# Optimization experiments

Hardware: AMD Instinct MI355X
Metric: run time of the kernel (lower is better)

## Reference

```python
import jax, jax.numpy as jnp
import numpy as np

HEAD = 12
HEAD_DIM = 64  # dim // head = 768 // 12


def setup_inputs() -> dict:
    key = jax.random.key(0)
    k1, k2, k3 = jax.random.split(key, 3)
    B, N, D = 4, 2048, 768
    scale = 1.0 / np.sqrt(D)
    return {
        "x": jax.random.normal(k1, (B, N, D), dtype=jnp.float32),
        "w_qkv": jax.random.normal(k2, (D, 3 * D), dtype=jnp.float32) * scale,
        "w_proj": jax.random.normal(k3, (D, D), dtype=jnp.float32) * scale,
        "b_proj": jnp.zeros((D,), dtype=jnp.float32),
    }


def reference(x, w_qkv, w_proj, b_proj):
    B, N, D = x.shape
    qkv = x @ w_qkv  # [B, N, 3D]
    q, k, v = jnp.split(qkv, 3, axis=-1)
    # [B, H, N, k]
    def heads(t):
        return t.reshape(B, N, HEAD, HEAD_DIM).transpose(0, 2, 1, 3)
    q, k, v = heads(q), heads(k), heads(v)
    attn = jnp.einsum("bhnd,bhmd->bhnm", q, k) / jnp.sqrt(jnp.float32(HEAD_DIM))
    attn_prob = jax.nn.softmax(attn, axis=-1)  # dropout p=0.0 -> identity
    out = jnp.einsum("bhnm,bhmd->bhnd", attn_prob, v)
    out = out.transpose(0, 2, 1, 3).reshape(B, N, D)
    return out @ w_proj + b_proj
```

## Files before the change

kernel.cpp:

```cpp
#include <hip/hip_runtime.h>

typedef unsigned short u16;
typedef unsigned int u32;
typedef u16 u16x4 __attribute__((ext_vector_type(4)));
typedef u16 u16x8 __attribute__((ext_vector_type(8)));
typedef u32 u32x2 __attribute__((ext_vector_type(2)));
typedef u32 u32x4 __attribute__((ext_vector_type(4)));
typedef __bf16 bf16x8 __attribute__((ext_vector_type(8)));
typedef float f32x4 __attribute__((ext_vector_type(4)));
typedef float f32x16 __attribute__((ext_vector_type(16)));

#define MFMA16 __builtin_amdgcn_mfma_f32_16x16x32_bf16
#define MFMA32 __builtin_amdgcn_mfma_f32_32x32x16_bf16

__device__ __forceinline__ u16 f2bf(float f) {
  return __builtin_bit_cast(u16, (__bf16)f);
}

__device__ __forceinline__ u32 pk2bf(float a, float b) {
  return (u32)__builtin_bit_cast(u16, (__bf16)a) |
         ((u32)__builtin_bit_cast(u16, (__bf16)b) << 16);
}

__device__ __forceinline__ u32x2 swap32(u32 a, u32 b, int hi) {
#if __has_builtin(__builtin_amdgcn_permlane32_swap)
  (void)hi;
  return __builtin_amdgcn_permlane32_swap(a, b, false, false);
#else
  u32 sa = (u32)__shfl_xor((int)a, 32), sb = (u32)__shfl_xor((int)b, 32);
  u32x2 r;
  r[0] = hi ? sb : a;
  r[1] = hi ? b : sa;
  return r;
#endif
}

__device__ __forceinline__ void gload_lds16(const void* g, void* l) {
  __builtin_amdgcn_global_load_lds(
      (const __attribute__((address_space(1))) u32*)g,
      (__attribute__((address_space(3))) u32*)l, 16, 0, 0);
}

__global__ __launch_bounds__(256)
void prepass_kernel(const float* __restrict__ x, u16* __restrict__ xb,
                    const float* __restrict__ wq, u16* __restrict__ wqT,
                    const float* __restrict__ wp, u16* __restrict__ wpT) {
  __shared__ float t[32][33];
  const int bid = blockIdx.x, tid = threadIdx.x;
  if (bid < 6144) {
    const int i = bid * 256 + tid;
    float4 v = reinterpret_cast<const float4*>(x)[i];
    u16x4 o;
    o[0] = f2bf(v.x); o[1] = f2bf(v.y); o[2] = f2bf(v.z); o[3] = f2bf(v.w);
    reinterpret_cast<u16x4*>(xb)[i] = o;
    return;
  }
  const float* w;
  u16* wt;
  int N, b2;
  if (bid < 7872) { b2 = bid - 6144; w = wq; wt = wqT; N = 2304; }
  else            { b2 = bid - 7872; w = wp; wt = wpT; N = 768; }
  const int K = 768;
  const int bk = (b2 % 24) * 32, bn = (b2 / 24) * 32;
  const int xx = tid & 31, yy = tid >> 5;
#pragma unroll
  for (int j = 0; j < 32; j += 8)
    t[yy + j][xx] = w[(size_t)(bk + yy + j) * N + bn + xx];
  __syncthreads();
#pragma unroll
  for (int j = 0; j < 32; j += 8)
    wt[(size_t)(bn + yy + j) * K + bk + xx] = f2bf(t[xx][yy + j]);
}

#define QSCALE 0.18033688011112042f

template <int NTOT, int EPI, int NT>
__global__ __launch_bounds__(256)
void gemm_bf16_kernel(const u16* __restrict__ A, const u16* __restrict__ BT,
                      u16* __restrict__ qo, u16* __restrict__ ko,
                      u16* __restrict__ vt, float* __restrict__ outF,
                      const float* __restrict__ bias) {
  __shared__ u16 sh[16384];
  u16* As = sh;
  u16* Bs = sh + 8192;
  const int tid = threadIdx.x;
  const int l = tid & 63, w = tid >> 6;
  const int lr = l & 15, lg = l >> 4;
  const int swz = (blockIdx.x & 7) * (8 * NT) + (blockIdx.x >> 3);
  const int mtile = swz / NT;
  const int ntile = swz % NT;
  const int mbase = mtile * 128, nbase = ntile * 128;
  const int wr = (w >> 1) * 64, wc = (w & 1) * 64;

  f32x4 acc[4][4] = {};

  for (int k0 = 0; k0 < 768; k0 += 64) {
#pragma unroll
    for (int i = 0; i < 4; ++i) {
      const int c = w * 64 + i * 256 + l;
      const int row = c >> 3, c16 = c & 7;
      const int sc = c16 ^ (row & 7);
      gload_lds16(A + (size_t)(mbase + row) * 768 + k0 + sc * 8,
                  &As[(size_t)(w * 64 + i * 256) * 8]);
      gload_lds16(BT + (size_t)(nbase + row) * 768 + k0 + sc * 8,
                  &Bs[(size_t)(w * 64 + i * 256) * 8]);
    }
    __syncthreads();
#pragma unroll
    for (int ks = 0; ks < 2; ++ks) {
      bf16x8 af[4], bfr[4];
#pragma unroll
      for (int m = 0; m < 4; ++m) {
        const int row = wr + m * 16 + lr;
        const int byte = (row * 128 + ks * 64 + lg * 16) ^ ((row & 7) << 4);
        af[m] = *reinterpret_cast<const bf16x8*>((const char*)As + byte);
      }
#pragma unroll
      for (int n = 0; n < 4; ++n) {
        const int row = wc + n * 16 + lr;
        const int byte = (row * 128 + ks * 64 + lg * 16) ^ ((row & 7) << 4);
        bfr[n] = *reinterpret_cast<const bf16x8*>((const char*)Bs + byte);
      }
#pragma unroll
      for (int m = 0; m < 4; ++m)
#pragma unroll
        for (int n = 0; n < 4; ++n)
          acc[m][n] = MFMA16(af[m], bfr[n], acc[m][n], 0, 0, 0);
    }
    __syncthreads();
  }

  if (EPI == 0 && ntile >= 12) {
    u16* vts = sh;
#pragma unroll
    for (int m = 0; m < 4; ++m)
#pragma unroll
      for (int n = 0; n < 4; ++n)
#pragma unroll
        for (int r = 0; r < 4; ++r) {
          const int col = wc + n * 16 + lr;
          const int row = wr + m * 16 + lg * 4 + r;
          const int byte = col * 256 + ((row * 2) ^ ((col & 7) << 4));
          *reinterpret_cast<u16*>((char*)vts + byte) = f2bf(acc[m][n][r]);
        }
    __syncthreads();
    const int b2 = mbase >> 11, nn0 = mbase & 2047;
#pragma unroll
    for (int i = 0; i < 8; ++i) {
      const int idx = i * 256 + tid;
      const int col = idx >> 4, u = idx & 15;
      u16x8 vv = *reinterpret_cast<u16x8*>(
          (char*)vts + (col * 256 + ((u * 16) ^ ((col & 7) << 4))));
      const int cg = nbase - 1536 + col;
      const int hh = cg >> 6, dd = cg & 63;
      *reinterpret_cast<u16x8*>(
          vt + (((size_t)(b2 * 12 + hh)) * 64 + dd) * 2048 + nn0 + u * 8) = vv;
    }
    return;
  }

#pragma unroll
  for (int m = 0; m < 4; ++m) {
#pragma unroll
    for (int n = 0; n < 4; ++n) {
#pragma unroll
      for (int r = 0; r < 4; ++r) {
        const int row = mbase + wr + m * 16 + lg * 4 + r;
        const int col = nbase + wc + n * 16 + lr;
        float val = acc[m][n][r];
        if (EPI == 0) {
          const int w2 = col / 768;
          const int c2 = col - w2 * 768;
          const int hh = c2 >> 6, dd = c2 & 63;
          const int b2 = row >> 11, nn = row & 2047;
          u16* dst = (w2 == 0) ? qo : ko;
          if (w2 == 0) val *= QSCALE;
          dst[(((size_t)(b2 * 12 + hh)) * 2048 + nn) * 64 + dd] = f2bf(val);
        } else {
          outF[(size_t)row * NTOT + col] = val + bias[col];
        }
      }
    }
  }
}

__global__ __launch_bounds__(256)
void flash_attn32_kernel(const u16* __restrict__ qb, const u16* __restrict__ kb,
                         const u16* __restrict__ vtb, u16* __restrict__ ao) {
  __shared__ u16 sh[32768];
  const int tid = threadIdx.x, w = tid >> 6, l = tid & 63;
  const int q5 = l & 31, hi = l >> 5;
  const int swz = (blockIdx.x & 7) * 96 + (blockIdx.x >> 3);
  const int bh = swz >> 4, qt = swz & 15;
  const int b = bh / 12, h = bh % 12;
  const int qrow0 = qt * 128 + w * 32;
  const u16* Q = qb + ((size_t)bh * 2048 + qrow0) * 64;
  const u16* K = kb + (size_t)bh * 2048 * 64;
  const u16* Vg = vtb + (size_t)bh * 64 * 2048;

  bf16x8 qf[4];
#pragma unroll
  for (int dk = 0; dk < 4; ++dk)
    qf[dk] = *reinterpret_cast<const bf16x8*>(Q + (size_t)q5 * 64 + dk * 16 + hi * 8);

  f32x16 ot0 = {}, ot1 = {};
  float l_ = 0.f;

  auto stage2 = [&](u16* base, int kt0) {
#pragma unroll
    for (int s = 0; s < 2; ++s) {
      u16* sb = base + s * 8192;
      const int kt = kt0 + s * 64;
#pragma unroll
      for (int i = 0; i < 2; ++i) {
        const int c = w * 64 + i * 256 + l;
        const int L = c >> 4, C = (c & 15) ^ (L & 15);
        const int row = L + ((C >> 3) << 5);
        gload_lds16(K + (size_t)(kt + row) * 64 + (C & 7) * 8,
                    sb + (size_t)(w * 64 + i * 256) * 8);
      }
#pragma unroll
      for (int i = 0; i < 2; ++i) {
        const int c = w * 64 + i * 256 + l;
        const int L = c >> 4, C = (c & 15) ^ (L & 15);
        const int d = L + ((C >> 3) << 5);
        gload_lds16(Vg + (size_t)d * 2048 + kt + (C & 7) * 8,
                    sb + 4096 + (size_t)(w * 64 + i * 256) * 8);
      }
    }
  };

  stage2(sh, 0);
  int cur = 0;
  const int q15 = q5 & 15;

  for (int win = 0; win < 16; ++win) {
    u16* tb = sh + cur * 16384;
    __builtin_amdgcn_sched_barrier(0);
    __builtin_amdgcn_s_barrier();
    __builtin_amdgcn_sched_barrier(0);
    if (win + 1 < 16) {
      stage2(sh + (cur ^ 1) * 16384, (win + 1) * 128);
      asm volatile("s_waitcnt vmcnt(8)" ::: "memory");
    } else {
      asm volatile("s_waitcnt vmcnt(0)" ::: "memory");
    }
    __builtin_amdgcn_sched_barrier(0);
    __builtin_amdgcn_s_barrier();
    __builtin_amdgcn_sched_barrier(0);

    const char* ksbA = (const char*)tb;
    const char* vsbA = (const char*)(tb + 4096);
    const char* ksbB = (const char*)(tb + 8192);
    const char* vsbB = (const char*)(tb + 12288);

    f32x16 sA0 = {}, sA1 = {}, sB0 = {}, sB1 = {};
    __builtin_amdgcn_s_setprio(1);
#pragma unroll
    for (int dk = 0; dk < 4; ++dk) {
      const int C = dk * 2 + hi;
      const int o0 = (C ^ q15) << 4, o1 = (((C + 8) ^ q15)) << 4;
      bf16x8 ka0 = *reinterpret_cast<const bf16x8*>(ksbA + q5 * 256 + o0);
      bf16x8 ka1 = *reinterpret_cast<const bf16x8*>(ksbA + q5 * 256 + o1);
      bf16x8 kb0 = *reinterpret_cast<const bf16x8*>(ksbB + q5 * 256 + o0);
      bf16x8 kb1 = *reinterpret_cast<const bf16x8*>(ksbB + q5 * 256 + o1);
      sA0 = MFMA32(ka0, qf[dk], sA0, 0, 0, 0);
      sA1 = MFMA32(ka1, qf[dk], sA1, 0, 0, 0);
      sB0 = MFMA32(kb0, qf[dk], sB0, 0, 0, 0);
      sB1 = MFMA32(kb1, qf[dk], sB1, 0, 0, 0);
    }
    __builtin_amdgcn_s_setprio(0);

    float lsA = 0.f, lsB = 0.f;
#pragma unroll
    for (int r = 0; r < 16; ++r) {
      sA0[r] = __builtin_amdgcn_exp2f(sA0[r]); lsA += sA0[r];
    }
#pragma unroll
    for (int r = 0; r < 16; ++r) {
      sA1[r] = __builtin_amdgcn_exp2f(sA1[r]); lsA += sA1[r];
    }
#pragma unroll
    for (int r = 0; r < 16; ++r) {
      sB0[r] = __builtin_amdgcn_exp2f(sB0[r]); lsB += sB0[r];
    }
#pragma unroll
    for (int r = 0; r < 16; ++r) {
      sB1[r] = __builtin_amdgcn_exp2f(sB1[r]); lsB += sB1[r];
    }
    l_ += lsA + __shfl_xor(lsA, 32);

    __builtin_amdgcn_s_setprio(1);
#pragma unroll
    for (int kvs = 0; kvs < 4; ++kvs) {
      const f32x16& stx = (kvs < 2) ? sA0 : sA1;
      const int rb = (kvs & 1) * 8;
      const u32 A0 = pk2bf(stx[rb + 0], stx[rb + 1]);
      const u32 A1 = pk2bf(stx[rb + 2], stx[rb + 3]);
      const u32 A2 = pk2bf(stx[rb + 4], stx[rb + 5]);
      const u32 A3 = pk2bf(stx[rb + 6], stx[rb + 7]);
      const u32x2 p02 = swap32(A0, A2, hi);
      const u32x2 p13 = swap32(A1, A3, hi);
      u32x4 wv;
      wv[0] = p02[0]; wv[1] = p13[0]; wv[2] = p02[1]; wv[3] = p13[1];
      const bf16x8 pf = __builtin_bit_cast(bf16x8, wv);
      const int Cv = kvs * 2 + hi;
      bf16x8 vf0 = *reinterpret_cast<const bf16x8*>(
          vsbA + q5 * 256 + ((Cv ^ q15) << 4));
      bf16x8 vf1 = *reinterpret_cast<const bf16x8*>(
          vsbA + q5 * 256 + (((Cv + 8) ^ q15) << 4));
      ot0 = MFMA32(vf0, pf, ot0, 0, 0, 0);
      ot1 = MFMA32(vf1, pf, ot1, 0, 0, 0);
    }
    __builtin_amdgcn_s_setprio(0);
    l_ += lsB + __shfl_xor(lsB, 32);
    __builtin_amdgcn_s_setprio(1);
#pragma unroll
    for (int kvs = 0; kvs < 4; ++kvs) {
      const f32x16& stx = (kvs < 2) ? sB0 : sB1;
      const int rb = (kvs & 1) * 8;
      const u32 A0 = pk2bf(stx[rb + 0], stx[rb + 1]);
      const u32 A1 = pk2bf(stx[rb + 2], stx[rb + 3]);
      const u32 A2 = pk2bf(stx[rb + 4], stx[rb + 5]);
      const u32 A3 = pk2bf(stx[rb + 6], stx[rb + 7]);
      const u32x2 p02 = swap32(A0, A2, hi);
      const u32x2 p13 = swap32(A1, A3, hi);
      u32x4 wv;
      wv[0] = p02[0]; wv[1] = p13[0]; wv[2] = p02[1]; wv[3] = p13[1];
      const bf16x8 pf = __builtin_bit_cast(bf16x8, wv);
      const int Cv = kvs * 2 + hi;
      bf16x8 vf0 = *reinterpret_cast<const bf16x8*>(
          vsbB + q5 * 256 + ((Cv ^ q15) << 4));
      bf16x8 vf1 = *reinterpret_cast<const bf16x8*>(
          vsbB + q5 * 256 + (((Cv + 8) ^ q15) << 4));
      ot0 = MFMA32(vf0, pf, ot0, 0, 0, 0);
      ot1 = MFMA32(vf1, pf, ot1, 0, 0, 0);
    }
    __builtin_amdgcn_s_setprio(0);
    cur ^= 1;
  }

  u16* ob = sh + w * 2048;
  const float inv = 1.0f / l_;
  const int swo = (q5 & 7) << 4;
#pragma unroll
  for (int g = 0; g < 4; ++g) {
    u16x4 pk0, pk1;
#pragma unroll
    for (int r = 0; r < 4; ++r) {
      pk0[r] = f2bf(ot0[g * 4 + r] * inv);
      pk1[r] = f2bf(ot1[g * 4 + r] * inv);
    }
    const int d0 = hi * 4 + g * 8;
    *reinterpret_cast<u16x4*>((char*)ob + ((q5 * 128 + d0 * 2) ^ swo)) = pk0;
    *reinterpret_cast<u16x4*>((char*)ob + ((q5 * 128 + (d0 + 32) * 2) ^ swo)) = pk1;
  }
  __syncthreads();
#pragma unroll
  for (int i = 0; i < 4; ++i) {
    const int idx = i * 64 + l;
    const int qr = idx >> 3, cc = idx & 7;
    u16x8 vv = *reinterpret_cast<u16x8*>(
        (char*)ob + ((qr * 128 + cc * 16) ^ ((qr & 7) << 4)));
    *reinterpret_cast<u16x8*>(
        ao + ((size_t)(b * 2048 + qrow0 + qr)) * 768 + h * 64 + cc * 8) = vv;
  }
}

extern "C" void kernel_launch(void* const* d_in, const int* in_sizes, int n_in,
                              void* d_out, int out_size, void* d_ws,
                              size_t ws_size, hipStream_t stream) {
  const float* x = (const float*)d_in[0];
  const float* w_qkv = (const float*)d_in[1];
  const float* w_proj = (const float*)d_in[2];
  const float* b_proj = (const float*)d_in[3];
  float* out = (float*)d_out;

  char* ws = (char*)d_ws;
  size_t off = 0;
  auto alloc = [&](size_t bytes) {
    char* p = ws + off;
    off += (bytes + 255) & ~(size_t)255;
    return p;
  };
  u16* xb = (u16*)alloc(8192ull * 768 * 2);
  u16* wqkvT = (u16*)alloc(2304ull * 768 * 2);
  u16* wprojT = (u16*)alloc(768ull * 768 * 2);
  u16* qbuf = (u16*)alloc(48ull * 2048 * 64 * 2);
  u16* kbuf = (u16*)alloc(48ull * 2048 * 64 * 2);
  u16* vtb = (u16*)alloc(48ull * 64 * 2048 * 2);
  u16* aob = (u16*)alloc(8192ull * 768 * 2);
  (void)ws_size; (void)n_in; (void)in_sizes; (void)out_size;

  prepass_kernel<<<8448, 256, 0, stream>>>(x, xb, w_qkv, wqkvT, w_proj, wprojT);

  gemm_bf16_kernel<2304, 0, 18><<<64 * 18, 256, 0, stream>>>(
      xb, wqkvT, qbuf, kbuf, vtb, nullptr, nullptr);

  flash_attn32_kernel<<<768, 256, 0, stream>>>(qbuf, kbuf, vtb, aob);

  gemm_bf16_kernel<768, 1, 6><<<64 * 6, 256, 0, stream>>>(
      aob, wprojT, nullptr, nullptr, nullptr, out, b_proj);
}
```

Before: 151.7 us.

## Split K and V staging into a three-slot rotating LDS pipeline

The attention kernel now stages K and V tiles separately across three rotating 16KB LDS slots, instead of double-buffering combined K+V tiles. This cuts shared memory from 64KB to 48KB per block, which may let more blocks fit on each CU. Each window now has two barriers: the next K load is issued before QK^T, and the next V load before PV, so both loads overlap with compute. After each waitcnt no barrier follows, so one wave may read LDS data another wave has not finished writing. That is a correctness risk.

```diff
diff --git a/kernel.cpp b/kernel.cpp
--- a/kernel.cpp
+++ b/kernel.cpp
@@ -187,7 +187,7 @@
 __global__ __launch_bounds__(256)
 void flash_attn32_kernel(const u16* __restrict__ qb, const u16* __restrict__ kb,
                          const u16* __restrict__ vtb, u16* __restrict__ ao) {
-  __shared__ u16 sh[32768];
+  __shared__ u16 sh[24576];
   const int tid = threadIdx.x, w = tid >> 6, l = tid & 63;
   const int q5 = l & 31, hi = l >> 5;
   const int swz = (blockIdx.x & 7) * 96 + (blockIdx.x >> 3);
@@ -206,10 +206,10 @@
   f32x16 ot0 = {}, ot1 = {};
   float l_ = 0.f;
 
-  auto stage2 = [&](u16* base, int kt0) {
+  auto stageK = [&](u16* slot, int kt0) {
 #pragma unroll
     for (int s = 0; s < 2; ++s) {
-      u16* sb = base + s * 8192;
+      u16* sb = slot + s * 4096;
       const int kt = kt0 + s * 64;
 #pragma unroll
       for (int i = 0; i < 2; ++i) {
@@ -219,40 +219,47 @@
         gload_lds16(K + (size_t)(kt + row) * 64 + (C & 7) * 8,
                     sb + (size_t)(w * 64 + i * 256) * 8);
       }
+    }
+  };
+  auto stageV = [&](u16* slot, int kt0) {
+#pragma unroll
+    for (int s = 0; s < 2; ++s) {
+      u16* sb = slot + s * 4096;
+      const int kt = kt0 + s * 64;
 #pragma unroll
       for (int i = 0; i < 2; ++i) {
         const int c = w * 64 + i * 256 + l;
         const int L = c >> 4, C = (c & 15) ^ (L & 15);
         const int d = L + ((C >> 3) << 5);
         gload_lds16(Vg + (size_t)d * 2048 + kt + (C & 7) * 8,
-                    sb + 4096 + (size_t)(w * 64 + i * 256) * 8);
+                    sb + (size_t)(w * 64 + i * 256) * 8);
       }
     }
   };
 
-  stage2(sh, 0);
-  int cur = 0;
+  stageK(sh, 0);
+  stageV(sh + 8192, 0);
+  int ksl = 0;
   const int q15 = q5 & 15;
 
   for (int win = 0; win < 16; ++win) {
-    u16* tb = sh + cur * 16384;
+    u16* kp = sh + ksl * 8192;
+    u16* vp = sh + ((ksl + 1) % 3) * 8192;
+    const int nksl = (ksl + 2) % 3;
+
     __builtin_amdgcn_sched_barrier(0);
     __builtin_amdgcn_s_barrier();
     __builtin_amdgcn_sched_barrier(0);
     if (win + 1 < 16) {
-      stage2(sh + (cur ^ 1) * 16384, (win + 1) * 128);
+      stageK(sh + nksl * 8192, (win + 1) * 128);
       asm volatile("s_waitcnt vmcnt(8)" ::: "memory");
     } else {
-      asm volatile("s_waitcnt vmcnt(0)" ::: "memory");
-    }
-    __builtin_amdgcn_sched_barrier(0);
-    __builtin_amdgcn_s_barrier();
-    __builtin_amdgcn_sched_barrier(0);
-
-    const char* ksbA = (const char*)tb;
-    const char* vsbA = (const char*)(tb + 4096);
-    const char* ksbB = (const char*)(tb + 8192);
-    const char* vsbB = (const char*)(tb + 12288);
+      asm volatile("s_waitcnt vmcnt(4)" ::: "memory");
+    }
+    __builtin_amdgcn_sched_barrier(0);
+
+    const char* ksbA = (const char*)kp;
+    const char* ksbB = (const char*)kp + 8192;
 
     f32x16 sA0 = {}, sA1 = {}, sB0 = {}, sB1 = {};
     __builtin_amdgcn_s_setprio(1);
@@ -270,6 +277,20 @@
       sB1 = MFMA32(kb1, qf[dk], sB1, 0, 0, 0);
     }
     __builtin_amdgcn_s_setprio(0);
+
+    __builtin_amdgcn_sched_barrier(0);
+    __builtin_amdgcn_s_barrier();
+    __builtin_amdgcn_sched_barrier(0);
+    if (win + 1 < 16) {
+      stageV(sh + ksl * 8192, (win + 1) * 128);
+      asm volatile("s_waitcnt vmcnt(8)" ::: "memory");
+    } else {
+      asm volatile("s_waitcnt vmcnt(0)" ::: "memory");
+    }
+    __builtin_amdgcn_sched_barrier(0);
+
+    const char* vsbA = (const char*)vp;
+    const char* vsbB = (const char*)vp + 8192;
 
     float lsA = 0.f, lsB = 0.f;
 #pragma unroll
@@ -337,8 +358,10 @@
       ot1 = MFMA32(vf1, pf, ot1, 0, 0, 0);
     }
     __builtin_amdgcn_s_setprio(0);
-    cur ^= 1;
-  }
+    ksl = nksl;
+  }
+
+  __syncthreads();
 
   u16* ob = sh + w * 2048;
   const float inv = 1.0f / l_;
```

After: 154.2 us. About the same (+1.6%).
